# Optimization experiments

Hardware: AMD Instinct MI355X
Metric: run time of the kernel (lower is better)

Reference implementation:

```python
import jax, jax.numpy as jnp
import numpy as np

N, D = 2, 256
M, L, K, DV = 8, 4, 4, 32
LK = L * K
LEVEL_HW = [(96, 96), (48, 48), (24, 24), (12, 12)]
S = sum(h * w for h, w in LEVEL_HW)  # 12240 flattened pyramid tokens
Q = S
OFFSET_SCALE = 0.5  # sampling_offset_scale_factor


def setup_inputs() -> dict:
    ks = jax.random.split(jax.random.key(0), 16)
    def lin(k, din, dout):
        return jax.random.normal(k, (din, dout), jnp.float32) / np.sqrt(din)
    return {
        "queries": jax.random.normal(ks[0], (N, Q, D), jnp.float32),
        "query_geometries": jax.random.uniform(ks[1], (N, Q, 4), jnp.float32, minval=0.1, maxval=0.9),
        "src_values": jax.random.normal(ks[2], (N, S, D), jnp.float32),
        "W_off": lin(ks[3], D, M * LK * 2) * 0.01,
        "b_off": jax.random.normal(ks[4], (M * LK * 2,), jnp.float32),
        "W_attn": lin(ks[5], D, M * LK),
        "b_attn": jnp.zeros((M * LK,), jnp.float32),
        "W_val": lin(ks[6], D, M * DV),
        "b_val": jnp.zeros((M * DV,), jnp.float32),
        "W_out": lin(ks[7], M * DV, D),
        "b_out": jnp.zeros((D,), jnp.float32),
    }


def _bilinear_sample(vmap_l, grid):
    # vmap_l: [B, dv, H, W]; grid: [B, Q, K, 2] in [-1, 1]
    # Matches F.grid_sample(mode='bilinear', align_corners=False, padding_mode='zeros')
    B, dv, H, W = vmap_l.shape
    x = (grid[..., 0] + 1.0) * (W / 2) - 0.5
    y = (grid[..., 1] + 1.0) * (H / 2) - 0.5
    x0 = jnp.floor(x)
    y0 = jnp.floor(y)
    wx = x - x0
    wy = y - y0
    x0i = x0.astype(jnp.int32)
    y0i = y0.astype(jnp.int32)
    vflat = vmap_l.reshape(B, dv, H * W)

    def corner(xi, yi, w):
        valid = (xi >= 0) & (xi < W) & (yi >= 0) & (yi < H)
        idx = jnp.clip(yi, 0, H - 1) * W + jnp.clip(xi, 0, W - 1)
        g = jax.vmap(lambda vf, i: vf[:, i])(vflat, idx)  # [B, dv, Q, K]
        return g * (w * valid)[:, None, :, :]

    return (corner(x0i, y0i, (1 - wx) * (1 - wy))
            + corner(x0i + 1, y0i, wx * (1 - wy))
            + corner(x0i, y0i + 1, (1 - wx) * wy)
            + corner(x0i + 1, y0i + 1, wx * wy))


def msdeform(queries, query_geometries, src_values, W_off, b_off, W_attn, b_attn,
             W_val, b_val, W_out, b_out):
    # attention weights: softmax over the L*K samples of each head
    attn = jax.nn.softmax((queries @ W_attn + b_attn).reshape(N, Q, M, LK), axis=-1)
    # predicted sampling offsets [N, Q, M, LK, 2]
    off = (queries @ W_off + b_off).reshape(N, Q, M, LK, 2)
    xy = query_geometries[..., :2]
    wh = query_geometries[..., 2:]
    scale = wh * (OFFSET_SCALE / K)  # wh * kv_count_per_level_inverse * sampling_offset_max_value
    pos = xy[:, :, None, None, :] + off * scale[:, :, None, None, :]  # normalized [0,1]
    # collapse (batch, head) -> B = N*M, rescale to [-1,1] for grid_sample semantics
    grid = (2.0 * pos - 1.0).transpose(0, 2, 1, 3, 4).reshape(N * M, Q, LK, 2)
    # project values and rebuild the per-level feature maps
    v = (src_values @ W_val + b_val).reshape(N, S, M, DV)
    samples, s = [], 0
    for l, (H, W) in enumerate(LEVEL_HW):
        vl = v[:, s:s + H * W].reshape(N, H, W, M, DV).transpose(0, 3, 4, 1, 2).reshape(N * M, DV, H, W)
        samples.append(_bilinear_sample(vl, grid[:, :, l * K:(l + 1) * K]))  # [N*M, DV, Q, K]
        s += H * W
    sampled = jnp.concatenate(samples, axis=-1)  # [N*M, DV, Q, LK]
    aw = attn.transpose(0, 2, 1, 3).reshape(N * M, 1, Q, LK)
    out = (sampled * aw).sum(-1)  # weighted reduction -> [N*M, DV, Q]
    out = out.reshape(N, M, DV, Q).transpose(0, 3, 1, 2).reshape(N, Q, M * DV)
    return out @ W_out + b_out  # backprojector


def reference(queries, query_geometries, src_values, W_off, b_off, W_attn, b_attn,
              W_val, b_val, W_out, b_out):
    return msdeform(queries, query_geometries, src_values, W_off, b_off, W_attn,
                    b_attn, W_val, b_val, W_out, b_out)
```

## Files before the change

### kernel.cpp

```cpp
#include <hip/hip_runtime.h>
#include <hip/hip_bf16.h>
#include <cstddef>

#define NB 2
#define QN 12240
#define SN 12240
#define MREAL 24480
#define MPAD  24576
#define MT    192

typedef unsigned short ushortT;
typedef unsigned int uintT;
typedef __bf16 bf16x8 __attribute__((ext_vector_type(8)));
typedef float f32x4 __attribute__((ext_vector_type(4)));

__device__ __forceinline__ ushortT f2bf(float f) {
    uintT u = __float_as_uint(f);
    uintT r = u + 0x7fffu + ((u >> 16) & 1u);
    return (ushortT)(r >> 16);
}
__device__ __forceinline__ float bf2f(ushortT u) {
    return __uint_as_float((uintT)u << 16);
}

__device__ __forceinline__ void async_ld16(const ushortT* g, ushortT* l) {
    __builtin_amdgcn_global_load_lds(
        (const __attribute__((address_space(1))) unsigned int*)g,
        (__attribute__((address_space(3))) unsigned int*)l, 16, 0, 0);
}

__global__ __launch_bounds__(256) void cast_qsrc(
    const float* __restrict__ q, const float* __restrict__ src,
    ushortT* __restrict__ qb, ushortT* __restrict__ sb)
{
    const size_t idx = ((size_t)blockIdx.x * 256 + threadIdx.x) * 8;
    if (idx >= (size_t)MREAL * 256) return;
    const float* in = (blockIdx.y == 0) ? q : src;
    ushortT* out = (blockIdx.y == 0) ? qb : sb;
    const float4 a = *(const float4*)(in + idx);
    const float4 b = *(const float4*)(in + idx + 4);
    uint4 o;
    o.x = (uintT)f2bf(a.x) | ((uintT)f2bf(a.y) << 16);
    o.y = (uintT)f2bf(a.z) | ((uintT)f2bf(a.w) << 16);
    o.z = (uintT)f2bf(b.x) | ((uintT)f2bf(b.y) << 16);
    o.w = (uintT)f2bf(b.z) | ((uintT)f2bf(b.w) << 16);
    *(uint4*)(out + idx) = o;
}

__global__ __launch_bounds__(256) void cast_weights(
    const float* __restrict__ Wval, const float* __restrict__ Wattn,
    const float* __restrict__ Woff, const float* __restrict__ Wout,
    ushortT* __restrict__ tval, ushortT* __restrict__ tlo,
    ushortT* __restrict__ tout)
{
    const int bx = blockIdx.x;
    const float* W; ushortT* T; int n, Nw, trow;
    if (bx < 256)      { W = Wval;  T = tval; n = bx;       Nw = 256; trow = n; }
    else if (bx < 384) { W = Wattn; T = tlo;  n = bx - 256; Nw = 128; trow = n; }
    else if (bx < 640) { W = Woff;  T = tlo;  n = bx - 384; Nw = 256; trow = n + 128; }
    else               { W = Wout;  T = tout; n = bx - 640; Nw = 256; trow = n; }
    const int k = threadIdx.x;
    T[(size_t)trow * 256 + k] = f2bf(W[(size_t)k * Nw + n]);
}

__global__ __launch_bounds__(256) void gemm_vlo(
    const ushortT* __restrict__ q_bf, const ushortT* __restrict__ src_bf,
    const ushortT* __restrict__ wt_val, const ushortT* __restrict__ wt_lo,
    const float* __restrict__ b_val, const float* __restrict__ b_attn,
    const float* __restrict__ b_off,
    ushortT* __restrict__ v_bf, float* __restrict__ lo_ws)
{
    const int z = blockIdx.z;
    if (z == 0 && blockIdx.x >= 2) return;

    __shared__ __attribute__((aligned(16))) ushortT As[128 * 32];
    __shared__ __attribute__((aligned(16))) ushortT Bs[128 * 32];

    const ushortT* A  = z ? q_bf : src_bf;
    const ushortT* Bt = z ? wt_lo : wt_val;

    const int tid  = threadIdx.x;
    const int wave = tid >> 6;
    const int lane = tid & 63;
    const int row0 = blockIdx.y * 128;
    const int col0 = blockIdx.x * 128;
    const int wr = (wave >> 1) * 64;
    const int wc = (wave & 1) * 64;

    f32x4 acc[4][4];
    #pragma unroll
    for (int i = 0; i < 4; i++)
        #pragma unroll
        for (int j = 0; j < 4; j++)
            acc[i][j] = (f32x4)0.f;

    const int srow = (lane >> 2);
    const int sk8  = (lane & 3) * 8;

    for (int k0 = 0; k0 < 256; k0 += 32) {
        #pragma unroll
        for (int j = 0; j < 2; j++) {
            const int r = wave * 32 + j * 16;
            async_ld16(A  + (size_t)(row0 + r + srow) * 256 + k0 + sk8, &As[r * 32]);
            async_ld16(Bt + (size_t)(col0 + r + srow) * 256 + k0 + sk8, &Bs[r * 32]);
        }
        __syncthreads();

        bf16x8 af[4], bfr[4];
        const int mrow = lane & 15;
        const int kq   = (lane >> 4) * 8;
        #pragma unroll
        for (int i = 0; i < 4; i++) {
            af[i]  = *(const bf16x8*)&As[(wr + i * 16 + mrow) * 32 + kq];
            bfr[i] = *(const bf16x8*)&Bs[(wc + i * 16 + mrow) * 32 + kq];
        }
        #pragma unroll
        for (int i = 0; i < 4; i++)
            #pragma unroll
            for (int j = 0; j < 4; j++)
                acc[i][j] = __builtin_amdgcn_mfma_f32_16x16x32_bf16(
                    af[i], bfr[j], acc[i][j], 0, 0, 0);
        __syncthreads();
    }

    const int Ntot = z ? 384 : 256;
    const float* bp = z ? ((col0 < 128) ? b_attn : b_off) : b_val;
    const int cofs  = (z && col0 >= 128) ? 128 : 0;

    #pragma unroll
    for (int i = 0; i < 4; i++) {
        const int rbase = row0 + wr + i * 16 + ((lane >> 4) << 2);
        #pragma unroll
        for (int j = 0; j < 4; j++) {
            const int col = col0 + wc + j * 16 + (lane & 15);
            const float bb = bp[col - cofs];
            #pragma unroll
            for (int r = 0; r < 4; r++) {
                const int row = rbase + r;
                if (row < MREAL) {
                    const float val = acc[i][j][r] + bb;
                    if (z) lo_ws[(size_t)row * 384 + col] = val;
                    else   v_bf[(size_t)row * 256 + col] = f2bf(val);
                }
            }
        }
    }
}

__global__ __launch_bounds__(256) void gemm_out(
    const ushortT* __restrict__ A, const ushortT* __restrict__ Bt,
    const float* __restrict__ bias, float* __restrict__ C)
{
    __shared__ __attribute__((aligned(16))) ushortT As[128 * 32];
    __shared__ __attribute__((aligned(16))) ushortT Bs[128 * 32];

    const int tid  = threadIdx.x;
    const int wave = tid >> 6;
    const int lane = tid & 63;
    const int row0 = blockIdx.y * 128;
    const int col0 = blockIdx.x * 128;
    const int wr = (wave >> 1) * 64;
    const int wc = (wave & 1) * 64;

    f32x4 acc[4][4];
    #pragma unroll
    for (int i = 0; i < 4; i++)
        #pragma unroll
        for (int j = 0; j < 4; j++)
            acc[i][j] = (f32x4)0.f;

    const int srow = (lane >> 2);
    const int sk8  = (lane & 3) * 8;

    for (int k0 = 0; k0 < 256; k0 += 32) {
        #pragma unroll
        for (int j = 0; j < 2; j++) {
            const int r = wave * 32 + j * 16;
            async_ld16(A  + (size_t)(row0 + r + srow) * 256 + k0 + sk8, &As[r * 32]);
            async_ld16(Bt + (size_t)(col0 + r + srow) * 256 + k0 + sk8, &Bs[r * 32]);
        }
        __syncthreads();

        bf16x8 af[4], bfr[4];
        const int mrow = lane & 15;
        const int kq   = (lane >> 4) * 8;
        #pragma unroll
        for (int i = 0; i < 4; i++) {
            af[i]  = *(const bf16x8*)&As[(wr + i * 16 + mrow) * 32 + kq];
            bfr[i] = *(const bf16x8*)&Bs[(wc + i * 16 + mrow) * 32 + kq];
        }
        #pragma unroll
        for (int i = 0; i < 4; i++)
            #pragma unroll
            for (int j = 0; j < 4; j++)
                acc[i][j] = __builtin_amdgcn_mfma_f32_16x16x32_bf16(
                    af[i], bfr[j], acc[i][j], 0, 0, 0);
        __syncthreads();
    }

    #pragma unroll
    for (int i = 0; i < 4; i++) {
        const int rbase = row0 + wr + i * 16 + ((lane >> 4) << 2);
        #pragma unroll
        for (int j = 0; j < 4; j++) {
            const int col = col0 + wc + j * 16 + (lane & 15);
            const float bb = bias[col];
            #pragma unroll
            for (int r = 0; r < 4; r++) {
                const int row = rbase + r;
                if (row < MREAL)
                    C[(size_t)row * 256 + col] = acc[i][j][r] + bb;
            }
        }
    }
}

__global__ __launch_bounds__(256) void sample_kernel(
    const float* __restrict__ lo,
    const float* __restrict__ geom,
    const ushortT* __restrict__ v,
    ushortT* __restrict__ out)
{
    const int tid = threadIdx.x;
    const int n  = blockIdx.y;
    const int q0 = blockIdx.x << 2;
    const int qi = tid >> 6;
    const int m  = (tid >> 3) & 7;

    __shared__ __attribute__((aligned(16))) int pls[32 * 132];

    {
        const int p = tid & 7;
        const size_t qb = (size_t)n * QN + q0 + qi;
        const float* lorow = lo + qb * 384;
        const float2 lg = *(const float2*)(lorow + m * 16 + p * 2);
        const float4 of = *(const float4*)(lorow + 128 + m * 32 + p * 4);
        const float4 g  = *(const float4*)(geom + qb * 4);

        float mx = fmaxf(lg.x, lg.y);
        mx = fmaxf(mx, __shfl_xor(mx, 1));
        mx = fmaxf(mx, __shfl_xor(mx, 2));
        mx = fmaxf(mx, __shfl_xor(mx, 4));
        const float e0 = __expf(lg.x - mx);
        const float e1 = __expf(lg.y - mx);
        float s = e0 + e1;
        s += __shfl_xor(s, 1);
        s += __shfl_xor(s, 2);
        s += __shfl_xor(s, 4);
        const float inv = 1.f / s;

        const int l  = p >> 1;
        const int Wl = 96 >> l;
        const int s0 = (l == 0) ? 0 : (l == 1) ? 9216 : (l == 2) ? 11520 : 12096;
        const float cx = g.x, cy = g.y;
        const float sx = g.z * 0.125f, sy = g.w * 0.125f;
        const int base = (qi * 8 + m) * 132 + p * 16;

        #pragma unroll
        for (int t = 0; t < 2; t++) {
            const float ox = t ? of.z : of.x;
            const float oy = t ? of.w : of.y;
            const float wa = (t ? e1 : e0) * inv;

            const float x = (cx + ox * sx) * (float)Wl - 0.5f;
            const float y = (cy + oy * sy) * (float)Wl - 0.5f;
            const float xf = floorf(x), yf = floorf(y);
            const int x0 = (int)xf, y0 = (int)yf;
            const float wx = x - xf, wy = y - yf;

            const bool vx0 = (x0 >= 0) & (x0 < Wl);
            const bool vx1 = (x0 + 1 >= 0) & (x0 + 1 < Wl);
            const bool vy0 = (y0 >= 0) & (y0 < Wl);
            const bool vy1 = (y0 + 1 >= 0) & (y0 + 1 < Wl);

            float4 wv;
            wv.x = (vx0 & vy0) ? wa * (1.f - wx) * (1.f - wy) : 0.f;
            wv.y = (vx1 & vy0) ? wa * wx * (1.f - wy) : 0.f;
            wv.z = (vx0 & vy1) ? wa * (1.f - wx) * wy : 0.f;
            wv.w = (vx1 & vy1) ? wa * wx * wy : 0.f;

            const int xc0 = min(max(x0, 0), Wl - 1);
            const int xc1 = min(max(x0 + 1, 0), Wl - 1);
            const int yc0 = min(max(y0, 0), Wl - 1);
            const int yc1 = min(max(y0 + 1, 0), Wl - 1);

            int4 iv;
            iv.x = (s0 + yc0 * Wl + xc0) << 9;
            iv.y = (s0 + yc0 * Wl + xc1) << 9;
            iv.z = (s0 + yc1 * Wl + xc0) << 9;
            iv.w = (s0 + yc1 * Wl + xc1) << 9;

            *(int4*)&pls[base + t * 8]       = iv;
            *(float4*)&pls[base + t * 8 + 4] = wv;
        }
    }
    __syncthreads();

    const int c = tid & 7;
    const int chan_byte = (m * 32 + c * 4) * 2;
    const unsigned char* vb = (const unsigned char*)(v + (size_t)n * SN * 256);
    const int gbase = (qi * 8 + m) * 132;

    float4 acc = make_float4(0.f, 0.f, 0.f, 0.f);

    #pragma unroll
    for (int lk = 0; lk < 16; lk++) {
        const int4   iv = *(const int4*)&pls[gbase + lk * 8];
        const float4 w  = *(const float4*)&pls[gbase + lk * 8 + 4];

        const ushort4 u00 = *(const ushort4*)(vb + (size_t)(iv.x + chan_byte));
        const ushort4 u10 = *(const ushort4*)(vb + (size_t)(iv.y + chan_byte));
        const ushort4 u01 = *(const ushort4*)(vb + (size_t)(iv.z + chan_byte));
        const ushort4 u11 = *(const ushort4*)(vb + (size_t)(iv.w + chan_byte));

        acc.x += w.x * bf2f(u00.x) + w.y * bf2f(u10.x) + w.z * bf2f(u01.x) + w.w * bf2f(u11.x);
        acc.y += w.x * bf2f(u00.y) + w.y * bf2f(u10.y) + w.z * bf2f(u01.y) + w.w * bf2f(u11.y);
        acc.z += w.x * bf2f(u00.z) + w.y * bf2f(u10.z) + w.z * bf2f(u01.z) + w.w * bf2f(u11.z);
        acc.w += w.x * bf2f(u00.w) + w.y * bf2f(u10.w) + w.z * bf2f(u01.w) + w.w * bf2f(u11.w);
    }

    ushort4 o;
    o.x = f2bf(acc.x); o.y = f2bf(acc.y); o.z = f2bf(acc.z); o.w = f2bf(acc.w);
    const size_t qb = (size_t)n * QN + q0 + qi;
    *(ushort4*)(out + qb * 256 + m * 32 + c * 4) = o;
}

extern "C" void kernel_launch(void* const* d_in, const int* in_sizes, int n_in,
                              void* d_out, int out_size, void* d_ws, size_t ws_size,
                              hipStream_t stream)
{
    const float* queries = (const float*)d_in[0];
    const float* geom    = (const float*)d_in[1];
    const float* src     = (const float*)d_in[2];
    const float* b_off   = (const float*)d_in[4];
    const float* W_off   = (const float*)d_in[3];
    const float* W_attn  = (const float*)d_in[5];
    const float* b_attn  = (const float*)d_in[6];
    const float* W_val   = (const float*)d_in[7];
    const float* b_val   = (const float*)d_in[8];
    const float* W_out   = (const float*)d_in[9];
    const float* b_out   = (const float*)d_in[10];
    float* out = (float*)d_out;

    ushortT* wsb = (ushortT*)d_ws;
    const size_t PADROW = (size_t)MPAD * 256;
    ushortT* q_bf    = wsb;
    ushortT* srcmdv  = wsb + PADROW;
    ushortT* v_bf    = wsb + 2 * PADROW;
    ushortT* wt_val  = wsb + 3 * PADROW;
    ushortT* wt_lo   = wt_val + 65536;
    ushortT* wt_out  = wt_lo + 98304;
    float* lo_ws = (float*)(wt_out + 65536);

    dim3 blk(256);

    cast_qsrc<<<dim3(3060, 2), blk, 0, stream>>>(queries, src, q_bf, srcmdv);
    cast_weights<<<dim3(896), blk, 0, stream>>>(
        W_val, W_attn, W_off, W_out, wt_val, wt_lo, wt_out);

    gemm_vlo<<<dim3(3, MT, 2), blk, 0, stream>>>(
        q_bf, srcmdv, wt_val, wt_lo, b_val, b_attn, b_off, v_bf, lo_ws);

    sample_kernel<<<dim3(QN / 4, NB), blk, 0, stream>>>(
        lo_ws, geom, v_bf, srcmdv);

    gemm_out<<<dim3(2, MT), blk, 0, stream>>>(srcmdv, wt_out, b_out, out);
}
```

Before: 214.4 us.

## Merge cast kernels, flatten value/proj GEMM grid, compact sampling records

The two cast kernels become one launch, and the combined value/projection GEMM grid drops its z dimension so no blocks exit early. In the sampling kernel each per-sample record shrinks from eight to four ints: a base offset, packed x/y corner deltas and half-precision bilinear weights. Corner loads use uint2 with a cheaper bf16 unpack. This cuts launch overhead, idle blocks, shared-memory traffic and address arithmetic, at the cost of fp16 precision on the attention-times-bilinear weights.

```diff
diff --git a/kernel.cpp b/kernel.cpp
--- a/kernel.cpp
+++ b/kernel.cpp
@@ -1,5 +1,6 @@
 #include <hip/hip_runtime.h>
 #include <hip/hip_bf16.h>
+#include <hip/hip_fp16.h>
 #include <cstddef>
 
 #define NB 2
@@ -19,8 +20,11 @@
     uintT r = u + 0x7fffu + ((u >> 16) & 1u);
     return (ushortT)(r >> 16);
 }
-__device__ __forceinline__ float bf2f(ushortT u) {
-    return __uint_as_float((uintT)u << 16);
+__device__ __forceinline__ float bf_lo(uintT u) {
+    return __uint_as_float(u << 16);
+}
+__device__ __forceinline__ float bf_hi(uintT u) {
+    return __uint_as_float(u & 0xffff0000u);
 }
 
 __device__ __forceinline__ void async_ld16(const ushortT* g, ushortT* l) {
@@ -29,31 +33,31 @@
         (__attribute__((address_space(3))) unsigned int*)l, 16, 0, 0);
 }
 
-__global__ __launch_bounds__(256) void cast_qsrc(
+__global__ __launch_bounds__(256) void cast_all(
     const float* __restrict__ q, const float* __restrict__ src,
-    ushortT* __restrict__ qb, ushortT* __restrict__ sb)
-{
-    const size_t idx = ((size_t)blockIdx.x * 256 + threadIdx.x) * 8;
-    if (idx >= (size_t)MREAL * 256) return;
-    const float* in = (blockIdx.y == 0) ? q : src;
-    ushortT* out = (blockIdx.y == 0) ? qb : sb;
-    const float4 a = *(const float4*)(in + idx);
-    const float4 b = *(const float4*)(in + idx + 4);
-    uint4 o;
-    o.x = (uintT)f2bf(a.x) | ((uintT)f2bf(a.y) << 16);
-    o.y = (uintT)f2bf(a.z) | ((uintT)f2bf(a.w) << 16);
-    o.z = (uintT)f2bf(b.x) | ((uintT)f2bf(b.y) << 16);
-    o.w = (uintT)f2bf(b.z) | ((uintT)f2bf(b.w) << 16);
-    *(uint4*)(out + idx) = o;
-}
-
-__global__ __launch_bounds__(256) void cast_weights(
     const float* __restrict__ Wval, const float* __restrict__ Wattn,
     const float* __restrict__ Woff, const float* __restrict__ Wout,
+    ushortT* __restrict__ qb, ushortT* __restrict__ sb,
     ushortT* __restrict__ tval, ushortT* __restrict__ tlo,
     ushortT* __restrict__ tout)
 {
-    const int bx = blockIdx.x;
+    int bx = blockIdx.x;
+    if (bx < 6120) {
+        const int issrc = bx >= 3060;
+        const size_t idx = ((size_t)(bx - (issrc ? 3060 : 0)) * 256 + threadIdx.x) * 8;
+        const float* in = issrc ? src : q;
+        ushortT* out = issrc ? sb : qb;
+        const float4 a = *(const float4*)(in + idx);
+        const float4 b = *(const float4*)(in + idx + 4);
+        uint4 o;
+        o.x = (uintT)f2bf(a.x) | ((uintT)f2bf(a.y) << 16);
+        o.y = (uintT)f2bf(a.z) | ((uintT)f2bf(a.w) << 16);
+        o.z = (uintT)f2bf(b.x) | ((uintT)f2bf(b.y) << 16);
+        o.w = (uintT)f2bf(b.z) | ((uintT)f2bf(b.w) << 16);
+        *(uint4*)(out + idx) = o;
+        return;
+    }
+    bx -= 6120;
     const float* W; ushortT* T; int n, Nw, trow;
     if (bx < 256)      { W = Wval;  T = tval; n = bx;       Nw = 256; trow = n; }
     else if (bx < 384) { W = Wattn; T = tlo;  n = bx - 256; Nw = 128; trow = n; }
@@ -70,8 +74,8 @@
     const float* __restrict__ b_off,
     ushortT* __restrict__ v_bf, float* __restrict__ lo_ws)
 {
-    const int z = blockIdx.z;
-    if (z == 0 && blockIdx.x >= 2) return;
+    const int z = blockIdx.x >= 2;
+    const int col0 = (z ? blockIdx.x - 2 : blockIdx.x) * 128;
 
     __shared__ __attribute__((aligned(16))) ushortT As[128 * 32];
     __shared__ __attribute__((aligned(16))) ushortT Bs[128 * 32];
@@ -83,7 +87,6 @@
     const int wave = tid >> 6;
     const int lane = tid & 63;
     const int row0 = blockIdx.y * 128;
-    const int col0 = blockIdx.x * 128;
     const int wr = (wave >> 1) * 64;
     const int wc = (wave & 1) * 64;
 
@@ -123,7 +126,6 @@
         __syncthreads();
     }
 
-    const int Ntot = z ? 384 : 256;
     const float* bp = z ? ((col0 < 128) ? b_attn : b_off) : b_val;
     const int cofs  = (z && col0 >= 128) ? 128 : 0;
 
@@ -221,17 +223,19 @@
     const ushortT* __restrict__ v,
     ushortT* __restrict__ out)
 {
-    const int tid = threadIdx.x;
-    const int n  = blockIdx.y;
-    const int q0 = blockIdx.x << 2;
-    const int qi = tid >> 6;
-    const int m  = (tid >> 3) & 7;
-
-    __shared__ __attribute__((aligned(16))) int pls[32 * 132];
+    const int tid  = threadIdx.x;
+    const int w    = tid >> 6;
+    const int lane = tid & 63;
+    const int m    = lane >> 3;
+    const int n    = blockIdx.y;
+    const int q0   = blockIdx.x << 2;
+
+    __shared__ __attribute__((aligned(16))) int pls[4][544];
+
+    const size_t qb = (size_t)n * QN + q0 + w;
 
     {
-        const int p = tid & 7;
-        const size_t qb = (size_t)n * QN + q0 + qi;
+        const int p = lane & 7;
         const float* lorow = lo + qb * 384;
         const float2 lg = *(const float2*)(lorow + m * 16 + p * 2);
         const float4 of = *(const float4*)(lorow + 128 + m * 32 + p * 4);
@@ -254,7 +258,7 @@
         const int s0 = (l == 0) ? 0 : (l == 1) ? 9216 : (l == 2) ? 11520 : 12096;
         const float cx = g.x, cy = g.y;
         const float sx = g.z * 0.125f, sy = g.w * 0.125f;
-        const int base = (qi * 8 + m) * 132 + p * 16;
+        int* myrec = &pls[w][m * 68 + p * 8];
 
         #pragma unroll
         for (int t = 0; t < 2; t++) {
@@ -273,55 +277,64 @@
             const bool vy0 = (y0 >= 0) & (y0 < Wl);
             const bool vy1 = (y0 + 1 >= 0) & (y0 + 1 < Wl);
 
-            float4 wv;
-            wv.x = (vx0 & vy0) ? wa * (1.f - wx) * (1.f - wy) : 0.f;
-            wv.y = (vx1 & vy0) ? wa * wx * (1.f - wy) : 0.f;
-            wv.z = (vx0 & vy1) ? wa * (1.f - wx) * wy : 0.f;
-            wv.w = (vx1 & vy1) ? wa * wx * wy : 0.f;
+            const float w00 = (vx0 & vy0) ? wa * (1.f - wx) * (1.f - wy) : 0.f;
+            const float w10 = (vx1 & vy0) ? wa * wx * (1.f - wy) : 0.f;
+            const float w01 = (vx0 & vy1) ? wa * (1.f - wx) * wy : 0.f;
+            const float w11 = (vx1 & vy1) ? wa * wx * wy : 0.f;
 
             const int xc0 = min(max(x0, 0), Wl - 1);
             const int xc1 = min(max(x0 + 1, 0), Wl - 1);
             const int yc0 = min(max(y0, 0), Wl - 1);
             const int yc1 = min(max(y0 + 1, 0), Wl - 1);
 
-            int4 iv;
-            iv.x = (s0 + yc0 * Wl + xc0) << 9;
-            iv.y = (s0 + yc0 * Wl + xc1) << 9;
-            iv.z = (s0 + yc1 * Wl + xc0) << 9;
-            iv.w = (s0 + yc1 * Wl + xc1) << 9;
-
-            *(int4*)&pls[base + t * 8]       = iv;
-            *(float4*)&pls[base + t * 8 + 4] = wv;
+            const int iv0   = (s0 + yc0 * Wl + xc0) << 9;
+            const int dx    = (xc1 - xc0) << 9;
+            const int dyrow = ((yc1 - yc0) * Wl) << 9;
+            __half2 h01 = __floats2half2_rn(w00, w10);
+            __half2 h23 = __floats2half2_rn(w01, w11);
+            int4 rec;
+            rec.x = iv0;
+            rec.y = dx | (dyrow << 16);
+            rec.z = *reinterpret_cast<int*>(&h01);
+            rec.w = *reinterpret_cast<int*>(&h23);
+            *(int4*)(myrec + t * 4) = rec;
         }
     }
     __syncthreads();
 
-    const int c = tid & 7;
+    const int c = lane & 7;
     const int chan_byte = (m * 32 + c * 4) * 2;
-    const unsigned char* vb = (const unsigned char*)(v + (size_t)n * SN * 256);
-    const int gbase = (qi * 8 + m) * 132;
-
-    float4 acc = make_float4(0.f, 0.f, 0.f, 0.f);
+    const unsigned char* vb =
+        (const unsigned char*)(v + (size_t)n * SN * 256);
+    const int* grec = &pls[w][m * 68];
+
+    float a0 = 0.f, a1 = 0.f, a2 = 0.f, a3 = 0.f;
 
     #pragma unroll
     for (int lk = 0; lk < 16; lk++) {
-        const int4   iv = *(const int4*)&pls[gbase + lk * 8];
-        const float4 w  = *(const float4*)&pls[gbase + lk * 8 + 4];
-
-        const ushort4 u00 = *(const ushort4*)(vb + (size_t)(iv.x + chan_byte));
-        const ushort4 u10 = *(const ushort4*)(vb + (size_t)(iv.y + chan_byte));
-        const ushort4 u01 = *(const ushort4*)(vb + (size_t)(iv.z + chan_byte));
-        const ushort4 u11 = *(const ushort4*)(vb + (size_t)(iv.w + chan_byte));
-
-        acc.x += w.x * bf2f(u00.x) + w.y * bf2f(u10.x) + w.z * bf2f(u01.x) + w.w * bf2f(u11.x);
-        acc.y += w.x * bf2f(u00.y) + w.y * bf2f(u10.y) + w.z * bf2f(u01.y) + w.w * bf2f(u11.y);
-        acc.z += w.x * bf2f(u00.z) + w.y * bf2f(u10.z) + w.z * bf2f(u01.z) + w.w * bf2f(u11.z);
-        acc.w += w.x * bf2f(u00.w) + w.y * bf2f(u10.w) + w.z * bf2f(u01.w) + w.w * bf2f(u11.w);
+        const int4 rec = *(const int4*)(grec + lk * 4);
+        const int base = rec.x + chan_byte;
+        const int dx   = rec.y & 0xffff;
+        const int dy   = ((uintT)rec.y) >> 16;
+
+        const uint2 u0 = *(const uint2*)(vb + base);
+        const uint2 u1 = *(const uint2*)(vb + base + dx);
+        const uint2 u2 = *(const uint2*)(vb + base + dy);
+        const uint2 u3 = *(const uint2*)(vb + base + dy + dx);
+
+        const __half2 h01 = *reinterpret_cast<const __half2*>(&rec.z);
+        const __half2 h23 = *reinterpret_cast<const __half2*>(&rec.w);
+        const float2 wlo = __half22float2(h01);
+        const float2 whi = __half22float2(h23);
+
+        a0 += wlo.x * bf_lo(u0.x) + wlo.y * bf_lo(u1.x) + whi.x * bf_lo(u2.x) + whi.y * bf_lo(u3.x);
+        a1 += wlo.x * bf_hi(u0.x) + wlo.y * bf_hi(u1.x) + whi.x * bf_hi(u2.x) + whi.y * bf_hi(u3.x);
+        a2 += wlo.x * bf_lo(u0.y) + wlo.y * bf_lo(u1.y) + whi.x * bf_lo(u2.y) + whi.y * bf_lo(u3.y);
+        a3 += wlo.x * bf_hi(u0.y) + wlo.y * bf_hi(u1.y) + whi.x * bf_hi(u2.y) + whi.y * bf_hi(u3.y);
     }
 
     ushort4 o;
-    o.x = f2bf(acc.x); o.y = f2bf(acc.y); o.z = f2bf(acc.z); o.w = f2bf(acc.w);
-    const size_t qb = (size_t)n * QN + q0 + qi;
+    o.x = f2bf(a0); o.y = f2bf(a1); o.z = f2bf(a2); o.w = f2bf(a3);
     *(ushort4*)(out + qb * 256 + m * 32 + c * 4) = o;
 }
 
@@ -332,8 +345,8 @@
     const float* queries = (const float*)d_in[0];
     const float* geom    = (const float*)d_in[1];
     const float* src     = (const float*)d_in[2];
+    const float* W_off   = (const float*)d_in[3];
     const float* b_off   = (const float*)d_in[4];
-    const float* W_off   = (const float*)d_in[3];
     const float* W_attn  = (const float*)d_in[5];
     const float* b_attn  = (const float*)d_in[6];
     const float* W_val   = (const float*)d_in[7];
@@ -354,11 +367,11 @@
 
     dim3 blk(256);
 
-    cast_qsrc<<<dim3(3060, 2), blk, 0, stream>>>(queries, src, q_bf, srcmdv);
-    cast_weights<<<dim3(896), blk, 0, stream>>>(
-        W_val, W_attn, W_off, W_out, wt_val, wt_lo, wt_out);
-
-    gemm_vlo<<<dim3(3, MT, 2), blk, 0, stream>>>(
+    cast_all<<<dim3(7016), blk, 0, stream>>>(
+        queries, src, W_val, W_attn, W_off, W_out,
+        q_bf, srcmdv, wt_val, wt_lo, wt_out);
+
+    gemm_vlo<<<dim3(5, MT), blk, 0, stream>>>(
         q_bf, srcmdv, wt_val, wt_lo, b_val, b_attn, b_off, v_bf, lo_ws);
 
     sample_kernel<<<dim3(QN / 4, NB), blk, 0, stream>>>(
```

Result: faster. 208.0 us (-3.0%).
